# Optimization experiments

Hardware: AMD Instinct MI355X
Metric: run time of the kernel (lower is better)

Reference implementation:

```python
import jax, jax.numpy as jnp
import numpy as np

B, T_PLUS_2, H, K = 128, 2050, 64, 100
BETA = 1.0


def setup_inputs() -> dict:
    key = jax.random.key(0)
    ks = jax.random.split(key, 7)
    event_tensor = jax.random.randint(ks[0], (B, T_PLUS_2), 0, K)            # fine event types
    dtime_tensor = jax.random.uniform(ks[1], (B, T_PLUS_2), dtype=jnp.float32)
    scale = 1.0 / np.sqrt(H)
    in_emb = jax.random.normal(ks[2], (K + 3, H), dtype=jnp.float32) * scale  # +BOS/EOS/PAD rows
    Wx = jax.random.normal(ks[3], (H, 7 * H), dtype=jnp.float32) * scale      # input -> 7 gates
    Wh = jax.random.normal(ks[4], (H, 7 * H), dtype=jnp.float32) * scale      # hidden -> 7 gates
    b = jnp.zeros((7 * H,), dtype=jnp.float32)
    out_emb = jax.random.normal(ks[5], (K, H), dtype=jnp.float32) * scale     # coarse-type embeddings
    return {"event_tensor": event_tensor, "dtime_tensor": dtime_tensor,
            "in_emb": in_emb, "Wx": Wx, "Wh": Wh, "b": b, "out_emb": out_emb}


def _ctlstm_intensities(event_tensor, dtime_tensor, in_emb, Wx, Wh, b, out_emb):
    # Embed input events for steps 0..T (drop last token): [B, T+1, H]
    emb = in_emb[event_tensor[:, :-1]]
    # Precompute the input-dependent part of all 7 gates outside the scan.
    pre = jnp.einsum('bth,hg->btg', emb, Wx) + b        # [B, T+1, 7H]
    dt = dtime_tensor[:, 1:]                            # [B, T+1] dtime to next event

    batch = event_tensor.shape[0]
    h_dim = in_emb.shape[1]
    init = (jnp.zeros((batch, h_dim), jnp.float32),     # c(t_i-)
            jnp.zeros((batch, h_dim), jnp.float32),     # cell_bar
            jnp.zeros((batch, h_dim), jnp.float32))     # h(t_i-)

    def step(carry, inp):
        c_minus, cb_prev, h_minus = carry
        pre_t, dt_t = inp                               # [B,7H], [B]
        g = pre_t + h_minus @ Wh
        gi, gf, gz, go, gib, gfb, gd = jnp.split(g, 7, axis=-1)
        i = jax.nn.sigmoid(gi)
        f = jax.nn.sigmoid(gf)
        z = jnp.tanh(gz)
        o = jax.nn.sigmoid(go)
        i_bar = jax.nn.sigmoid(gib)
        f_bar = jax.nn.sigmoid(gfb)
        delta = jax.nn.softplus(gd)
        c_i = f * c_minus + i * z
        cb_i = f_bar * cb_prev + i_bar * z
        # decay over the interval dt: c(t)=cb+(c-cb)exp(-delta dt), h=o*tanh(c)
        c_next = cb_i + (c_i - cb_i) * jnp.exp(-delta * dt_t[:, None])
        h_next = o * jnp.tanh(c_next)
        return (c_next, cb_i, h_next), h_next

    _, hs = jax.lax.scan(step, init, (pre.transpose(1, 0, 2), dt.T))
    hs = hs.transpose(1, 0, 2)                          # [B, T+1, H] hidden at t_{i+1}^-
    # softplus with beta: (1/beta) * softplus(beta * x); identity fine<->coarse map
    logits = jnp.einsum('bth,kh->btk', hs, out_emb)
    return jax.nn.softplus(BETA * logits) / BETA        # [B, T+1, K]


def reference(event_tensor, dtime_tensor, in_emb, Wx, Wh, b, out_emb):
    return _ctlstm_intensities(event_tensor, dtime_tensor, in_emb, Wx, Wh, b, out_emb)
```

## Files before the change

kernel.cpp:

```cpp
#include <hip/hip_runtime.h>
#include <math.h>

#define BB 128
#define T2 2050
#define TT 2049
#define HH 64
#define GG 448
#define KK 100
#define NE 103
#define NSTAGE 2056
#define NTHREADS 576

#define LOG2E 1.44269504088896340736f
#define LN2   0.69314718055994530942f

__device__ __forceinline__ float frcp(float x) { return __builtin_amdgcn_rcpf(x); }

__device__ __forceinline__ float sigmoid_fast(float x) {
    return frcp(1.f + exp2f(-x * LOG2E));
}
__device__ __forceinline__ float tanh_fast(float x) {
    float e = exp2f(x * (2.f * LOG2E));
    return 1.f - 2.f * frcp(1.f + e);
}
__device__ __forceinline__ float softplus_fast(float x) {
    float t = exp2f(-fabsf(x) * LOG2E);
    return fmaxf(x, 0.f) + LN2 * log2f(1.f + t);
}

__global__ void pre_emb_kernel(const float* __restrict__ in_emb,
                               const float* __restrict__ Wx,
                               const float* __restrict__ bias,
                               float* __restrict__ pre_emb) {
    int e = blockIdx.x;
    int t = threadIdx.x;
    float acc = bias[t];
#pragma unroll
    for (int k = 0; k < HH; ++k)
        acc = fmaf(in_emb[e * HH + k], Wx[k * GG + t], acc);
    pre_emb[e * GG + t] = acc;
}

__device__ __forceinline__ void step_barrier() {
    __builtin_amdgcn_sched_barrier(0);
    asm volatile("s_waitcnt lgkmcnt(0)" ::: "memory");
    __builtin_amdgcn_s_barrier();
    __builtin_amdgcn_sched_barrier(0);
}

__launch_bounds__(NTHREADS, 1)
__global__ void scan_kernel(const int* __restrict__ event,
                            const float* __restrict__ dtime,
                            const float* __restrict__ pre_emb,
                            const float* __restrict__ Wh,
                            const float* __restrict__ oe,
                            float* __restrict__ out) {
    const int b   = blockIdx.x;
    const int tid = threadIdx.x;
    const int w   = tid >> 6;
    const int l   = tid & 63;
    const int h2  = l >> 5;
    const int s5  = l & 31;

    __shared__ float gbuf[2][7][HH];
    __shared__ __align__(16) float h_sw[7][2][HH];
    __shared__ int   evoff_s[NSTAGE];
    __shared__ float dtl_s[NSTAGE];

    const bool is_gate = (w < 7);
    const int  jw      = w - 7;

    const int*   ev_row  = event + b * T2;
    const float* dt_row  = dtime + b * T2;
    float*       out_row = out + (size_t)b * TT * KK;

    for (int i = tid; i < NSTAGE; i += NTHREADS) {
        const int idx = (i < T2) ? i : (T2 - 1);
        evoff_s[i] = ev_row[idx] * GG;
        dtl_s[i]   = dt_row[idx];
    }

    float wA[32], wB[32];
    if (is_gate) {
        const int cA = w * 64 + s5;
        const int cB = w * 64 + 32 + s5;
#pragma unroll
        for (int kk = 0; kk < 32; ++kk) {
            const int k = 32 * h2 + kk;
            wA[kk] = Wh[k * GG + cA];
            wB[kk] = Wh[k * GG + cB];
        }
    } else {
        int cA = 64 * jw + s5;       if (cA > KK - 1) cA = KK - 1;
        int cB = 64 * jw + 32 + s5;  if (cB > KK - 1) cB = KK - 1;
#pragma unroll
        for (int j = 0; j < 8; ++j) {
            ((float4*)wA)[j] = ((const float4*)(oe + cA * HH + 32 * h2))[j];
            ((float4*)wB)[j] = ((const float4*)(oe + cB * HH + 32 * h2))[j];
        }
    }

    __syncthreads();

    const int colOff = w * 64 + 32 * h2 + s5;
    float preE = 0.f, preO = 0.f, dtE = 0.f, dtO = 0.f;
    int   offE = 0, offO = 0;
    if (is_gate) {
        const float p0  = pre_emb[evoff_s[0] + colOff];
        const float dt0 = dtl_s[1];
        float v0;
        if (w == 2)      v0 = tanh_fast(p0);
        else if (w == 6) v0 = exp2f(-dt0 * log2f(1.f + exp2f(p0 * LOG2E)));
        else             v0 = sigmoid_fast(p0);
        gbuf[0][w][32 * h2 + s5] = v0;

        preE = pre_emb[evoff_s[1] + colOff];
        preO = pre_emb[evoff_s[2] + colOff];
        offE = evoff_s[3];
        offO = evoff_s[4];
        dtE  = dtl_s[2];
        dtO  = dtl_s[3];
    }
    __syncthreads();

    float c = 0.f, cb = 0.f;

    const int  lcolA = 64 * jw + s5;
    const int  lcolB = 64 * jw + 32 + s5;
    float*     outP  = out_row;

#define GATE_STEP(RB, WB, PRE, OFF, DTV, TIDX)                                  \
    {                                                                           \
        const float pre_use = PRE;                                              \
        PRE = pre_emb[OFF + colOff];                \
        OFF = evoff_s[(TIDX) + 5];                                              \
        const float dt_use = DTV;                                               \
        DTV = dtl_s[(TIDX) + 4];                                                \
                \
        const float g0 = gbuf[RB][0][l];                                        \
        const float g1 = gbuf[RB][1][l];                                        \
        const float g2 = gbuf[RB][2][l];                                        \
        const float g3 = gbuf[RB][3][l];                                        \
        const float g4 = gbuf[RB][4][l];                                        \
        const float g5 = gbuf[RB][5][l];                                        \
        const float g6 = gbuf[RB][6][l];        \
        const float ci  = fmaf(g1, c, g0 * g2);                                 \
        const float cbi = fmaf(g5, cb, g4 * g2);                                \
        const float cn  = fmaf(ci - cbi, g6, cbi);                              \
        const float h   = g3 * tanh_fast(cn);                                   \
        c  = cn;                                                                \
        cb = cbi;                                                               \
        h_sw[w][RB][l] = h;                                                     \
                     \
        const float4* h4 = (const float4*)&h_sw[w][RB][32 * h2];                \
        float pA = 0.f, pB = 0.f;                                               \
        _Pragma("unroll") for (int j = 0; j < 8; ++j) {                         \
            const float4 hv = h4[j];                                            \
            pA = fmaf(hv.x, wA[4 * j + 0], pA);                                 \
            pB = fmaf(hv.x, wB[4 * j + 0], pB);                                 \
            pA = fmaf(hv.y, wA[4 * j + 1], pA);                                 \
            pB = fmaf(hv.y, wB[4 * j + 1], pB);                                 \
            pA = fmaf(hv.z, wA[4 * j + 2], pA);                                 \
            pB = fmaf(hv.z, wB[4 * j + 2], pB);                                 \
            pA = fmaf(hv.w, wA[4 * j + 3], pA);                                 \
            pB = fmaf(hv.w, wB[4 * j + 3], pB);                                 \
        }                                                                       \
        pA += __shfl_xor(pA, 32);                                               \
        pB += __shfl_xor(pB, 32);                                               \
        const float acc = pre_use + (h2 ? pB : pA);                             \
        float val;                                                              \
        if (w == 2)      val = tanh_fast(acc);                                  \
        else if (w == 6) val = exp2f(-dt_use * log2f(1.f + exp2f(acc * LOG2E)));\
        else             val = sigmoid_fast(acc);                               \
        gbuf[WB][w][32 * h2 + s5] = val;                                        \
    }

#define LOGIT_STEP(HB, DO_STORE)                                                \
    {                                                                           \
        const float4* h4 = (const float4*)&h_sw[0][HB][32 * h2];                \
        float pA = 0.f, pB = 0.f;                                               \
        _Pragma("unroll") for (int j = 0; j < 8; ++j) {                         \
            const float4 hv = h4[j];                                            \
            pA = fmaf(hv.x, wA[4 * j + 0], pA);                                 \
            pB = fmaf(hv.x, wB[4 * j + 0], pB);                                 \
            pA = fmaf(hv.y, wA[4 * j + 1], pA);                                 \
            pB = fmaf(hv.y, wB[4 * j + 1], pB);                                 \
            pA = fmaf(hv.z, wA[4 * j + 2], pA);                                 \
            pB = fmaf(hv.z, wB[4 * j + 2], pB);                                 \
            pA = fmaf(hv.w, wA[4 * j + 3], pA);                                 \
            pB = fmaf(hv.w, wB[4 * j + 3], pB);                                 \
        }                                                                       \
        pA += __shfl_xor(pA, 32);                                               \
        pB += __shfl_xor(pB, 32);                                               \
        if (DO_STORE) {                                                         \
            const float lg  = h2 ? pB : pA;                                     \
            const int   col = h2 ? lcolB : lcolA;                               \
            if (col < KK) outP[col] = softplus_fast(lg);                        \
            outP += KK;                                                         \
        }                                                                       \
    }

    if (is_gate) __builtin_amdgcn_s_setprio(1);

    for (int tp = 0; tp < (TT - 1) / 2; ++tp) {
        const int te = 2 * tp;
        if (is_gate) { GATE_STEP(0, 1, preE, offE, dtE, te) }
        else         { LOGIT_STEP(1, (tp > 0)) }
        step_barrier();
        if (is_gate) { GATE_STEP(1, 0, preO, offO, dtO, te + 1) }
        else         { LOGIT_STEP(0, true) }
        step_barrier();
    }
    if (is_gate) { GATE_STEP(0, 1, preE, offE, dtE, TT - 1) }
    else         { LOGIT_STEP(1, true) }
    step_barrier();
    if (is_gate) __builtin_amdgcn_s_setprio(0);

    if (!is_gate) { LOGIT_STEP(0, true) }

#undef GATE_STEP
#undef LOGIT_STEP
}

extern "C" void kernel_launch(void* const* d_in, const int* in_sizes, int n_in,
                              void* d_out, int out_size, void* d_ws, size_t ws_size,
                              hipStream_t stream) {
    const int*   event  = (const int*)d_in[0];
    const float* dtime  = (const float*)d_in[1];
    const float* in_emb = (const float*)d_in[2];
    const float* Wx     = (const float*)d_in[3];
    const float* Wh     = (const float*)d_in[4];
    const float* bias   = (const float*)d_in[5];
    const float* oe     = (const float*)d_in[6];
    float*       out    = (float*)d_out;

    float* pre_emb = (float*)d_ws;

    pre_emb_kernel<<<NE, GG, 0, stream>>>(in_emb, Wx, bias, pre_emb);
    scan_kernel<<<BB, NTHREADS, 0, stream>>>(event, dtime, pre_emb, Wh, oe, out);
}
```

Measured before the change: 1.395 ms.

## Restructure scan so each gate thread computes all seven gates with k-split reduction

Replaces the layout of 7 gate waves plus 2 logit waves with 4 gate waves and 2 logit waves. Each gate thread now holds weights for all 7 gates over a 16-wide k-slice, reduces across four k-groups with permlane swap instructions, and applies the cell update locally. This removes the intermediate gate-buffer round trip through LDS, leaving one barrier per step instead of effectively two dependent phases. In exchange each thread does more serial FMA and transcendental work and uses many more registers (112 weights plus 64 for logits).

```diff
diff --git a/kernel.cpp b/kernel.cpp
--- a/kernel.cpp
+++ b/kernel.cpp
@@ -9,7 +9,7 @@
 #define KK 100
 #define NE 103
 #define NSTAGE 2056
-#define NTHREADS 576
+#define NTHREADS 384
 
 #define LOG2E 1.44269504088896340736f
 #define LN2   0.69314718055994530942f
@@ -26,6 +26,15 @@
 __device__ __forceinline__ float softplus_fast(float x) {
     float t = exp2f(-fabsf(x) * LOG2E);
     return fmaxf(x, 0.f) + LN2 * log2f(1.f + t);
+}
+
+__device__ __forceinline__ float ksum4(float v) {
+    float a = v, b = v;
+    asm("v_permlane16_swap_b32 %0, %1" : "+v"(a), "+v"(b));
+    float s = a + b;
+    float x = s, y = s;
+    asm("v_permlane32_swap_b32 %0, %1" : "+v"(x), "+v"(y));
+    return x + y;
 }
 
 __global__ void pre_emb_kernel(const float* __restrict__ in_emb,
@@ -59,16 +68,16 @@
     const int tid = threadIdx.x;
     const int w   = tid >> 6;
     const int l   = tid & 63;
-    const int h2  = l >> 5;
-    const int s5  = l & 31;
-
-    __shared__ float gbuf[2][7][HH];
-    __shared__ __align__(16) float h_sw[7][2][HH];
+    const int k4  = l >> 4;
+    const int c16 = l & 15;
+
+    __shared__ __align__(16) float hs[2][HH];
     __shared__ int   evoff_s[NSTAGE];
     __shared__ float dtl_s[NSTAGE];
 
-    const bool is_gate = (w < 7);
-    const int  jw      = w - 7;
+    const bool is_gate = (w < 4);
+    const int  jw      = w - 4;
+    const int  colb    = 16 * (w & 3) + c16;
 
     const int*   ev_row  = event + b * T2;
     const float* dt_row  = dtime + b * T2;
@@ -80,143 +89,165 @@
         dtl_s[i]   = dt_row[idx];
     }
 
-    float wA[32], wB[32];
+    float wg[7][16];
+    float wl[4][16];
     if (is_gate) {
-        const int cA = w * 64 + s5;
-        const int cB = w * 64 + 32 + s5;
-#pragma unroll
-        for (int kk = 0; kk < 32; ++kk) {
-            const int k = 32 * h2 + kk;
-            wA[kk] = Wh[k * GG + cA];
-            wB[kk] = Wh[k * GG + cB];
+#pragma unroll
+        for (int g = 0; g < 7; ++g)
+#pragma unroll
+            for (int kk = 0; kk < 16; ++kk)
+                wg[g][kk] = Wh[(16 * k4 + kk) * GG + g * 64 + colb];
+#pragma unroll
+        for (int g = 0; g < 7; ++g)
+#pragma unroll
+            for (int kk = 0; kk < 16; ++kk)
+                asm volatile("" : "+v"(wg[g][kk]));
+    } else {
+#pragma unroll
+        for (int j = 0; j < 4; ++j) {
+            const bool valid = (c16 + 16 * j) < 50;
+            const int  col   = valid ? (50 * jw + c16 + 16 * j) : (50 * jw);
+#pragma unroll
+            for (int kk = 0; kk < 16; ++kk)
+                wl[j][kk] = oe[col * HH + 16 * k4 + kk];
         }
-    } else {
-        int cA = 64 * jw + s5;       if (cA > KK - 1) cA = KK - 1;
-        int cB = 64 * jw + 32 + s5;  if (cB > KK - 1) cB = KK - 1;
-#pragma unroll
-        for (int j = 0; j < 8; ++j) {
-            ((float4*)wA)[j] = ((const float4*)(oe + cA * HH + 32 * h2))[j];
-            ((float4*)wB)[j] = ((const float4*)(oe + cB * HH + 32 * h2))[j];
+#pragma unroll
+        for (int j = 0; j < 4; ++j)
+#pragma unroll
+            for (int kk = 0; kk < 16; ++kk)
+                asm volatile("" : "+v"(wl[j][kk]));
+    }
+
+    if (tid < HH) hs[0][tid] = 0.f;
+    __syncthreads();
+
+    float preE[7], preO[7];
+    int   offE = 0, offO = 0;
+    float dtE = 0.f, dtO = 0.f;
+    if (is_gate) {
+        const int o0 = evoff_s[0], o1 = evoff_s[1];
+#pragma unroll
+        for (int g = 0; g < 7; ++g) {
+            preE[g] = pre_emb[o0 + g * 64 + colb];
+            preO[g] = pre_emb[o1 + g * 64 + colb];
         }
-    }
-
-    __syncthreads();
-
-    const int colOff = w * 64 + 32 * h2 + s5;
-    float preE = 0.f, preO = 0.f, dtE = 0.f, dtO = 0.f;
-    int   offE = 0, offO = 0;
-    if (is_gate) {
-        const float p0  = pre_emb[evoff_s[0] + colOff];
-        const float dt0 = dtl_s[1];
-        float v0;
-        if (w == 2)      v0 = tanh_fast(p0);
-        else if (w == 6) v0 = exp2f(-dt0 * log2f(1.f + exp2f(p0 * LOG2E)));
-        else             v0 = sigmoid_fast(p0);
-        gbuf[0][w][32 * h2 + s5] = v0;
-
-        preE = pre_emb[evoff_s[1] + colOff];
-        preO = pre_emb[evoff_s[2] + colOff];
-        offE = evoff_s[3];
-        offO = evoff_s[4];
-        dtE  = dtl_s[2];
-        dtO  = dtl_s[3];
-    }
-    __syncthreads();
+        offE = evoff_s[2];
+        offO = evoff_s[3];
+        dtE  = dtl_s[1];
+        dtO  = dtl_s[2];
+    }
 
     float c = 0.f, cb = 0.f;
 
-    const int  lcolA = 64 * jw + s5;
-    const int  lcolB = 64 * jw + 32 + s5;
-    float*     outP  = out_row;
+    const int  lc0 = 50 * jw + c16;
+    const int  lc1 = lc0 + 16;
+    const int  lc2 = lc0 + 32;
+    const int  lc3 = lc0 + 48;
+    float*     outP = out_row;
 
 #define GATE_STEP(RB, WB, PRE, OFF, DTV, TIDX)                                  \
     {                                                                           \
-        const float pre_use = PRE;                                              \
-        PRE = pre_emb[OFF + colOff];                \
-        OFF = evoff_s[(TIDX) + 5];                                              \
-        const float dt_use = DTV;                                               \
-        DTV = dtl_s[(TIDX) + 4];                                                \
-                \
-        const float g0 = gbuf[RB][0][l];                                        \
-        const float g1 = gbuf[RB][1][l];                                        \
-        const float g2 = gbuf[RB][2][l];                                        \
-        const float g3 = gbuf[RB][3][l];                                        \
-        const float g4 = gbuf[RB][4][l];                                        \
-        const float g5 = gbuf[RB][5][l];                                        \
-        const float g6 = gbuf[RB][6][l];        \
-        const float ci  = fmaf(g1, c, g0 * g2);                                 \
-        const float cbi = fmaf(g5, cb, g4 * g2);                                \
-        const float cn  = fmaf(ci - cbi, g6, cbi);                              \
-        const float h   = g3 * tanh_fast(cn);                                   \
+        float pu[7];                                                            \
+        _Pragma("unroll") for (int g = 0; g < 7; ++g) pu[g] = PRE[g];           \
+        const float* pb = pre_emb + OFF;                                        \
+        _Pragma("unroll") for (int g = 0; g < 7; ++g) PRE[g] = pb[g * 64 + colb]; \
+        OFF = evoff_s[(TIDX) + 4];                                              \
+        const float dtu = DTV;                                                  \
+        DTV = dtl_s[(TIDX) + 3];                                                \
+        const float4* hp = (const float4*)&hs[RB][16 * k4];                     \
+        const float4 hv0 = hp[0], hv1 = hp[1], hv2 = hp[2], hv3 = hp[3];        \
+        float acc[7];                                                           \
+        _Pragma("unroll") for (int g = 0; g < 7; ++g) {                         \
+            float a = hv0.x * wg[g][0];                                         \
+            a = fmaf(hv0.y, wg[g][1],  a);                                      \
+            a = fmaf(hv0.z, wg[g][2],  a);                                      \
+            a = fmaf(hv0.w, wg[g][3],  a);                                      \
+            a = fmaf(hv1.x, wg[g][4],  a);                                      \
+            a = fmaf(hv1.y, wg[g][5],  a);                                      \
+            a = fmaf(hv1.z, wg[g][6],  a);                                      \
+            a = fmaf(hv1.w, wg[g][7],  a);                                      \
+            a = fmaf(hv2.x, wg[g][8],  a);                                      \
+            a = fmaf(hv2.y, wg[g][9],  a);                                      \
+            a = fmaf(hv2.z, wg[g][10], a);                                      \
+            a = fmaf(hv2.w, wg[g][11], a);                                      \
+            a = fmaf(hv3.x, wg[g][12], a);                                      \
+            a = fmaf(hv3.y, wg[g][13], a);                                      \
+            a = fmaf(hv3.z, wg[g][14], a);                                      \
+            a = fmaf(hv3.w, wg[g][15], a);                                      \
+            acc[g] = a;                                                         \
+        }                                                                       \
+        float gate[7];                                                          \
+        _Pragma("unroll") for (int g = 0; g < 7; ++g)                           \
+            gate[g] = ksum4(acc[g]) + pu[g];                                    \
+        const float ed  = exp2f(-dtu * log2f(1.f + exp2f(gate[6] * LOG2E)));    \
+        const float zg  = tanh_fast(gate[2]);                                   \
+        const float ig  = sigmoid_fast(gate[0]);                                \
+        const float fg  = sigmoid_fast(gate[1]);                                \
+        const float ibg = sigmoid_fast(gate[4]);                                \
+        const float fbg = sigmoid_fast(gate[5]);                                \
+        const float og  = sigmoid_fast(gate[3]);                                \
+        const float ci  = fmaf(fg, c, ig * zg);                                 \
+        const float cbi = fmaf(fbg, cb, ibg * zg);                              \
+        const float cn  = fmaf(ci - cbi, ed, cbi);                              \
+        const float h   = og * tanh_fast(cn);                                   \
         c  = cn;                                                                \
         cb = cbi;                                                               \
-        h_sw[w][RB][l] = h;                                                     \
-                     \
-        const float4* h4 = (const float4*)&h_sw[w][RB][32 * h2];                \
-        float pA = 0.f, pB = 0.f;                                               \
-        _Pragma("unroll") for (int j = 0; j < 8; ++j) {                         \
-            const float4 hv = h4[j];                                            \
-            pA = fmaf(hv.x, wA[4 * j + 0], pA);                                 \
-            pB = fmaf(hv.x, wB[4 * j + 0], pB);                                 \
-            pA = fmaf(hv.y, wA[4 * j + 1], pA);                                 \
-            pB = fmaf(hv.y, wB[4 * j + 1], pB);                                 \
-            pA = fmaf(hv.z, wA[4 * j + 2], pA);                                 \
-            pB = fmaf(hv.z, wB[4 * j + 2], pB);                                 \
-            pA = fmaf(hv.w, wA[4 * j + 3], pA);                                 \
-            pB = fmaf(hv.w, wB[4 * j + 3], pB);                                 \
+        if (k4 == 0) hs[WB][colb] = h;                                          \
+    }
+
+#define LOGIT_STEP(RB, DO_STORE)                                                \
+    {                                                                           \
+        const float4* hp = (const float4*)&hs[RB][16 * k4];                     \
+        const float4 hv0 = hp[0], hv1 = hp[1], hv2 = hp[2], hv3 = hp[3];        \
+        float acc[4];                                                           \
+        _Pragma("unroll") for (int j = 0; j < 4; ++j) {                         \
+            float a = hv0.x * wl[j][0];                                         \
+            a = fmaf(hv0.y, wl[j][1],  a);                                      \
+            a = fmaf(hv0.z, wl[j][2],  a);                                      \
+            a = fmaf(hv0.w, wl[j][3],  a);                                      \
+            a = fmaf(hv1.x, wl[j][4],  a);                                      \
+            a = fmaf(hv1.y, wl[j][5],  a);                                      \
+            a = fmaf(hv1.z, wl[j][6],  a);                                      \
+            a = fmaf(hv1.w, wl[j][7],  a);                                      \
+            a = fmaf(hv2.x, wl[j][8],  a);                                      \
+            a = fmaf(hv2.y, wl[j][9],  a);                                      \
+            a = fmaf(hv2.z, wl[j][10], a);                                      \
+            a = fmaf(hv2.w, wl[j][11], a);                                      \
+            a = fmaf(hv3.x, wl[j][12], a);                                      \
+            a = fmaf(hv3.y, wl[j][13], a);                                      \
+            a = fmaf(hv3.z, wl[j][14], a);                                      \
+            a = fmaf(hv3.w, wl[j][15], a);                                      \
+            acc[j] = a;                                                         \
         }                                                                       \
-        pA += __shfl_xor(pA, 32);                                               \
-        pB += __shfl_xor(pB, 32);                                               \
-        const float acc = pre_use + (h2 ? pB : pA);                             \
-        float val;                                                              \
-        if (w == 2)      val = tanh_fast(acc);                                  \
-        else if (w == 6) val = exp2f(-dt_use * log2f(1.f + exp2f(acc * LOG2E)));\
-        else             val = sigmoid_fast(acc);                               \
-        gbuf[WB][w][32 * h2 + s5] = val;                                        \
-    }
-
-#define LOGIT_STEP(HB, DO_STORE)                                                \
-    {                                                                           \
-        const float4* h4 = (const float4*)&h_sw[0][HB][32 * h2];                \
-        float pA = 0.f, pB = 0.f;                                               \
-        _Pragma("unroll") for (int j = 0; j < 8; ++j) {                         \
-            const float4 hv = h4[j];                                            \
-            pA = fmaf(hv.x, wA[4 * j + 0], pA);                                 \
-            pB = fmaf(hv.x, wB[4 * j + 0], pB);                                 \
-            pA = fmaf(hv.y, wA[4 * j + 1], pA);                                 \
-            pB = fmaf(hv.y, wB[4 * j + 1], pB);                                 \
-            pA = fmaf(hv.z, wA[4 * j + 2], pA);                                 \
-            pB = fmaf(hv.z, wB[4 * j + 2], pB);                                 \
-            pA = fmaf(hv.w, wA[4 * j + 3], pA);                                 \
-            pB = fmaf(hv.w, wB[4 * j + 3], pB);                                 \
-        }                                                                       \
-        pA += __shfl_xor(pA, 32);                                               \
-        pB += __shfl_xor(pB, 32);                                               \
+        const float r0 = ksum4(acc[0]);                                         \
+        const float r1 = ksum4(acc[1]);                                         \
+        const float r2 = ksum4(acc[2]);                                         \
+        const float r3 = ksum4(acc[3]);                                         \
         if (DO_STORE) {                                                         \
-            const float lg  = h2 ? pB : pA;                                     \
-            const int   col = h2 ? lcolB : lcolA;                               \
-            if (col < KK) outP[col] = softplus_fast(lg);                        \
+            if (k4 == 0) {                                                      \
+                outP[lc0] = softplus_fast(r0);                                  \
+                outP[lc1] = softplus_fast(r1);                                  \
+                outP[lc2] = softplus_fast(r2);                                  \
+                if (c16 < 2) outP[lc3] = softplus_fast(r3);                     \
+            }                                                                   \
             outP += KK;                                                         \
         }                                                                       \
     }
-
-    if (is_gate) __builtin_amdgcn_s_setprio(1);
 
     for (int tp = 0; tp < (TT - 1) / 2; ++tp) {
         const int te = 2 * tp;
         if (is_gate) { GATE_STEP(0, 1, preE, offE, dtE, te) }
-        else         { LOGIT_STEP(1, (tp > 0)) }
+        else         { LOGIT_STEP(0, (te > 0)) }
         step_barrier();
         if (is_gate) { GATE_STEP(1, 0, preO, offO, dtO, te + 1) }
-        else         { LOGIT_STEP(0, true) }
+        else         { LOGIT_STEP(1, true) }
         step_barrier();
     }
     if (is_gate) { GATE_STEP(0, 1, preE, offE, dtE, TT - 1) }
-    else         { LOGIT_STEP(1, true) }
+    else         { LOGIT_STEP(0, true) }
     step_barrier();
-    if (is_gate) __builtin_amdgcn_s_setprio(0);
-
-    if (!is_gate) { LOGIT_STEP(0, true) }
+
+    if (!is_gate) { LOGIT_STEP(1, true) }
 
 #undef GATE_STEP
 #undef LOGIT_STEP
```

After: 1.899 ms. 1.36x slower.
